# Kernel optimization log

Measured on AMD Instinct MI355X. Metric: run time of the kernel, lower is better.

## Reference

```python
import jax, jax.numpy as jnp
import numpy as np

# Static taxonomy layout (closed over; mirrors __init__ args La/layers)
LAYER_SIZES = (100, 1000, 5000, 13900)
LAYER_STARTS = tuple(int(s) for s in np.cumsum((0,) + LAYER_SIZES)[:-1])
N_NODES = int(sum(LAYER_SIZES))
H = len(LAYER_SIZES)
BATCH = 4096


def setup_inputs() -> dict:
    key = jax.random.key(0)
    y_pred = jax.random.normal(key, (BATCH, N_NODES), dtype=jnp.float32)

    rng = np.random.default_rng(0)
    # parents[v] = global index of v's parent in the previous layer
    parents = np.zeros(N_NODES, np.int32)
    for l in range(1, H):
        s, n = LAYER_STARTS[l], LAYER_SIZES[l]
        ps, pn = LAYER_STARTS[l - 1], LAYER_SIZES[l - 1]
        parents[s:s + n] = rng.integers(ps, ps + pn, size=n)

    # hierarchy-consistent one-hot targets: pick a leaf, mark it and all ancestors
    leaf = rng.integers(LAYER_STARTS[H - 1], N_NODES, size=BATCH)
    y_true = np.zeros((BATCH, N_NODES), np.float32)
    node = leaf
    rows = np.arange(BATCH)
    for l in range(H - 1, 0, -1):
        y_true[rows, node] = 1.0
        node = parents[node]
    y_true[rows, node] = 1.0  # layer-0 ancestor

    alpha_layer = jnp.array([0.0, 1.0, 1.0, 1.0], dtype=jnp.float32)
    return {
        "y_pred": y_pred,
        "y_true": jnp.asarray(y_true),
        "parents": jnp.asarray(parents),
        "alpha_layer": alpha_layer,
    }


def reference(y_pred, y_true, parents, alpha_layer):
    # Fused, batched version of the per-sample / per-layer Python loops.
    loss = jnp.float32(0.0)
    for l in range(1, H):  # small static loop over taxonomy layers
        s, n = LAYER_STARTS[l], LAYER_SIZES[l]
        ps, pn = LAYER_STARTS[l - 1], LAYER_SIZES[l - 1]

        logits = y_pred[:, s:s + n]                      # [B, n_l]
        p = jax.nn.softmax(logits, axis=1)               # outer softmax (as in source)
        # nn.CrossEntropyLoss with probability targets == -sum(t * log_softmax(input));
        # the source feeds the already-softmaxed p (double softmax) -> reproduce exactly.
        cce = -jnp.sum(y_true[:, s:s + n] * jax.nn.log_softmax(p, axis=1), axis=1)  # [B]

        # hierarchical dependency: child prob must not exceed its parent's prob
        pp = jax.nn.softmax(y_pred[:, ps:ps + pn], axis=1)   # [B, n_{l-1}]
        pidx = parents[s:s + n] - ps                         # local parent ids [n_l]
        d = jnp.mean(jax.nn.relu(p - pp[:, pidx]), axis=1)   # [B]

        loss = loss + jnp.mean(cce + d) * alpha_layer[l]
    return loss
```

## Files before the change

kernel.cpp:

```cpp
#include <hip/hip_runtime.h>
#include <math.h>

#define BATCH   4096
#define N_NODES 20000
#define H       4
#define BLOCK   512
#define NW      (BLOCK / 64)

__device__ __forceinline__ float waveSum(float v) {
#pragma unroll
    for (int off = 32; off > 0; off >>= 1) v += __shfl_xor(v, off);
    return v;
}

__device__ __forceinline__ ushort f2bf(float x) {
    unsigned u = __float_as_uint(x);
    u = (u + 0x7FFFu + ((u >> 16) & 1u)) >> 16;
    return (ushort)u;
}
__device__ __forceinline__ float bf2f(ushort h) {
    return __uint_as_float(((unsigned)h) << 16);
}

__device__ __forceinline__ void mzMerge(float& m, float& z, float m2, float z2) {
    float mn = fmaxf(m, m2);
    z = z * __expf(m - mn) + z2 * __expf(m2 - mn);
    m = mn;
}

__global__ __launch_bounds__(BLOCK, 8) void tax_main(
    const float* __restrict__ y_pred,
    const float* __restrict__ y_true,
    const int*   __restrict__ parents,
    const float* __restrict__ alpha,
    float*       __restrict__ partial)
{
    constexpr int LSTART[H] = {0, 100, 1100, 6100};
    constexpr int LSIZE[H]  = {100, 1000, 5000, 13900};

    __shared__ __align__(8) ushort row_bf[N_NODES];
    __shared__ float sc[112];
    __shared__ float m_s[H], invZ_s[H];

    const int tid = threadIdx.x;
    const int b   = blockIdx.x;
    const int wid = tid >> 6;
    const int lid = tid & 63;

    const float4* src4 = reinterpret_cast<const float4*>(y_pred + (size_t)b * N_NODES);

    float mL[H], zL[H];
#pragma unroll
    for (int l = 0; l < H; ++l) { mL[l] = -1e30f; zL[l] = 0.f; }

#pragma unroll
    for (int l = 0; l < H; ++l) {
        const int sq = LSTART[l] / 4, nq = LSIZE[l] / 4;
        for (int i = tid; i < nq; i += BLOCK) {
            float4 v = src4[sq + i];
            ushort4 h;
            h.x = f2bf(v.x); h.y = f2bf(v.y); h.z = f2bf(v.z); h.w = f2bf(v.w);
            *reinterpret_cast<ushort4*>(&row_bf[4 * (sq + i)]) = h;
            float qm = fmaxf(fmaxf(v.x, v.y), fmaxf(v.z, v.w));
            float mn = fmaxf(mL[l], qm);
            zL[l] = zL[l] * __expf(mL[l] - mn)
                  + __expf(v.x - mn) + __expf(v.y - mn)
                  + __expf(v.z - mn) + __expf(v.w - mn);
            mL[l] = mn;
        }
    }

#pragma unroll
    for (int l = 0; l < H; ++l) {
#pragma unroll
        for (int off = 32; off > 0; off >>= 1) {
            float m2 = __shfl_xor(mL[l], off);
            float z2 = __shfl_xor(zL[l], off);
            mzMerge(mL[l], zL[l], m2, z2);
        }
    }
    if (lid == 0) {
#pragma unroll
        for (int l = 0; l < H; ++l) {
            sc[wid * 8 + l * 2]     = mL[l];
            sc[wid * 8 + l * 2 + 1] = zL[l];
        }
    }
    __syncthreads();
    if (tid < H) {
        float m = -1e30f, z = 0.f;
        for (int w = 0; w < NW; ++w)
            mzMerge(m, z, sc[w * 8 + tid * 2], sc[w * 8 + tid * 2 + 1]);
        m_s[tid]    = m;
        invZ_s[tid] = 1.f / z;
    }
    __syncthreads();

#pragma unroll
    for (int l = 1; l < H; ++l) {
        const int s = LSTART[l], nq = LSIZE[l] / 4;
        const float invZ  = invZ_s[l],     m  = m_s[l];
        const float invZp = invZ_s[l - 1], mp = m_s[l - 1];
        const float4* yt4 = reinterpret_cast<const float4*>(y_true + (size_t)b * N_NODES + s);
        const int4*   pa4 = reinterpret_cast<const int4*>(parents + s);

        float S = 0.f, dot = 0.f, D = 0.f, yts = 0.f;
        for (int i = tid; i < nq; i += BLOCK) {
            ushort4 yh = *reinterpret_cast<const ushort4*>(&row_bf[s + 4 * i]);
            float4  yt = yt4[i];
            int4    pa = pa4[i];
            float p0 = __expf(bf2f(yh.x) - m) * invZ;
            float p1 = __expf(bf2f(yh.y) - m) * invZ;
            float p2 = __expf(bf2f(yh.z) - m) * invZ;
            float p3 = __expf(bf2f(yh.w) - m) * invZ;
            float pp0 = __expf(bf2f(row_bf[pa.x]) - mp) * invZp;
            float pp1 = __expf(bf2f(row_bf[pa.y]) - mp) * invZp;
            float pp2 = __expf(bf2f(row_bf[pa.z]) - mp) * invZp;
            float pp3 = __expf(bf2f(row_bf[pa.w]) - mp) * invZp;
            S   += __expf(p0) + __expf(p1) + __expf(p2) + __expf(p3);
            dot += yt.x * p0 + yt.y * p1 + yt.z * p2 + yt.w * p3;
            yts += yt.x + yt.y + yt.z + yt.w;
            D += fmaxf(p0 - pp0, 0.f) + fmaxf(p1 - pp1, 0.f)
               + fmaxf(p2 - pp2, 0.f) + fmaxf(p3 - pp3, 0.f);
        }

        S = waveSum(S); dot = waveSum(dot); D = waveSum(D); yts = waveSum(yts);
        if (lid == 0) {
            sc[wid * 12 + (l - 1) * 4 + 0] = S;
            sc[wid * 12 + (l - 1) * 4 + 1] = dot;
            sc[wid * 12 + (l - 1) * 4 + 2] = D;
            sc[wid * 12 + (l - 1) * 4 + 3] = yts;
        }
    }
    __syncthreads();

    if (tid < 12) {
        float a = 0.f;
        for (int w = 0; w < NW; ++w) a += sc[w * 12 + tid];
        sc[96 + tid] = a;
    }
    __syncthreads();

    if (tid == 0) {
        float loss = 0.f;
#pragma unroll
        for (int l = 1; l < H; ++l) {
            float S   = sc[96 + (l - 1) * 4 + 0];
            float dot = sc[96 + (l - 1) * 4 + 1];
            float D   = sc[96 + (l - 1) * 4 + 2];
            float yts = sc[96 + (l - 1) * 4 + 3];
            loss += alpha[l] * (logf(S) * yts - dot + D / (float)LSIZE[l]);
        }
        partial[b] = loss;
    }
}

__global__ __launch_bounds__(1024) void tax_reduce(
    const float* __restrict__ partial, float* __restrict__ out)
{
    __shared__ float red[16];
    const int tid = threadIdx.x, wid = tid >> 6, lid = tid & 63;
    float v = 0.f;
    for (int i = tid; i < BATCH; i += 1024) v += partial[i];
    v = waveSum(v);
    if (lid == 0) red[wid] = v;
    __syncthreads();
    if (wid == 0) {
        float x = (lid < 16) ? red[lid] : 0.f;
        x = waveSum(x);
        if (lid == 0) out[0] = x * (1.0f / (float)BATCH);
    }
}

extern "C" void kernel_launch(void* const* d_in, const int* in_sizes, int n_in,
                              void* d_out, int out_size, void* d_ws, size_t ws_size,
                              hipStream_t stream) {
    const float* y_pred  = (const float*)d_in[0];
    const float* y_true  = (const float*)d_in[1];
    const int*   parents = (const int*)d_in[2];
    const float* alpha   = (const float*)d_in[3];
    float* partial = (float*)d_ws;
    float* out     = (float*)d_out;

    tax_main<<<dim3(BATCH), dim3(BLOCK), 0, stream>>>(y_pred, y_true, parents, alpha, partial);
    tax_reduce<<<dim3(1), dim3(1024), 0, stream>>>(partial, out);
}
```

Before: 130.1 us.

## Fold y_true dot product into first streaming pass with online rescaling

The y_true row is now read during the first pass over y_pred. The target-weighted dot product of unnormalized exponentials is accumulated with the same online max rescaling used for the softmax denominator, then multiplied by 1/Z at the end. This removes the y_true global reads and the dot/yts accumulation from the second pass, so that pass only reads shared memory and parents. The same DRAM bytes are still read, but they are issued earlier and together with y_pred loads. The cost is extra registers and extra multiply-adds in the first pass.

```diff
diff --git a/kernel.cpp b/kernel.cpp
--- a/kernel.cpp
+++ b/kernel.cpp
@@ -22,12 +22,6 @@
     return __uint_as_float(((unsigned)h) << 16);
 }
 
-__device__ __forceinline__ void mzMerge(float& m, float& z, float m2, float z2) {
-    float mn = fmaxf(m, m2);
-    z = z * __expf(m - mn) + z2 * __expf(m2 - mn);
-    m = mn;
-}
-
 __global__ __launch_bounds__(BLOCK, 8) void tax_main(
     const float* __restrict__ y_pred,
     const float* __restrict__ y_true,
@@ -39,75 +33,97 @@
     constexpr int LSIZE[H]  = {100, 1000, 5000, 13900};
 
     __shared__ __align__(8) ushort row_bf[N_NODES];
-    __shared__ float sc[112];
-    __shared__ float m_s[H], invZ_s[H];
+    __shared__ float sc[128];
+    __shared__ float fin[6];
+    __shared__ float m_s[H], invZ_s[H], dot_s[H], yts_s[H];
 
     const int tid = threadIdx.x;
     const int b   = blockIdx.x;
     const int wid = tid >> 6;
     const int lid = tid & 63;
 
-    const float4* src4 = reinterpret_cast<const float4*>(y_pred + (size_t)b * N_NODES);
+    const float4* yp4 = reinterpret_cast<const float4*>(y_pred + (size_t)b * N_NODES);
+    const float4* yt4 = reinterpret_cast<const float4*>(y_true + (size_t)b * N_NODES);
 
-    float mL[H], zL[H];
+    float mL[H], zL[H], dotL[H], ytsL[H];
 #pragma unroll
-    for (int l = 0; l < H; ++l) { mL[l] = -1e30f; zL[l] = 0.f; }
+    for (int l = 0; l < H; ++l) { mL[l] = -1e30f; zL[l] = 0.f; dotL[l] = 0.f; ytsL[l] = 0.f; }
 
 #pragma unroll
     for (int l = 0; l < H; ++l) {
         const int sq = LSTART[l] / 4, nq = LSIZE[l] / 4;
+        float m = mL[l], z = zL[l], dt = dotL[l], ys = ytsL[l];
         for (int i = tid; i < nq; i += BLOCK) {
-            float4 v = src4[sq + i];
+            float4 v = yp4[sq + i];
             ushort4 h;
             h.x = f2bf(v.x); h.y = f2bf(v.y); h.z = f2bf(v.z); h.w = f2bf(v.w);
             *reinterpret_cast<ushort4*>(&row_bf[4 * (sq + i)]) = h;
             float qm = fmaxf(fmaxf(v.x, v.y), fmaxf(v.z, v.w));
-            float mn = fmaxf(mL[l], qm);
-            zL[l] = zL[l] * __expf(mL[l] - mn)
-                  + __expf(v.x - mn) + __expf(v.y - mn)
-                  + __expf(v.z - mn) + __expf(v.w - mn);
-            mL[l] = mn;
+            float mn = fmaxf(m, qm);
+            float a  = __expf(m - mn);
+            float e0 = __expf(v.x - mn), e1 = __expf(v.y - mn);
+            float e2 = __expf(v.z - mn), e3 = __expf(v.w - mn);
+            z = z * a + (e0 + e1) + (e2 + e3);
+            if (l > 0) {
+                float4 t = yt4[sq + i];
+                dt = dt * a + t.x * e0 + t.y * e1 + t.z * e2 + t.w * e3;
+                ys += (t.x + t.y) + (t.z + t.w);
+            }
+            m = mn;
         }
+        mL[l] = m; zL[l] = z; dotL[l] = dt; ytsL[l] = ys;
     }
 
 #pragma unroll
     for (int l = 0; l < H; ++l) {
+        float m = mL[l], z = zL[l], dt = dotL[l], ys = ytsL[l];
 #pragma unroll
         for (int off = 32; off > 0; off >>= 1) {
-            float m2 = __shfl_xor(mL[l], off);
-            float z2 = __shfl_xor(zL[l], off);
-            mzMerge(mL[l], zL[l], m2, z2);
+            float m2 = __shfl_xor(m, off), z2 = __shfl_xor(z, off);
+            float d2 = __shfl_xor(dt, off), y2 = __shfl_xor(ys, off);
+            float mn = fmaxf(m, m2);
+            float aa = __expf(m - mn), bb = __expf(m2 - mn);
+            z = z * aa + z2 * bb;
+            dt = dt * aa + d2 * bb;
+            m = mn; ys += y2;
         }
-    }
-    if (lid == 0) {
-#pragma unroll
-        for (int l = 0; l < H; ++l) {
-            sc[wid * 8 + l * 2]     = mL[l];
-            sc[wid * 8 + l * 2 + 1] = zL[l];
+        if (lid == 0) {
+            sc[wid * 16 + l * 4 + 0] = m;
+            sc[wid * 16 + l * 4 + 1] = z;
+            sc[wid * 16 + l * 4 + 2] = dt;
+            sc[wid * 16 + l * 4 + 3] = ys;
         }
     }
     __syncthreads();
+
     if (tid < H) {
-        float m = -1e30f, z = 0.f;
-        for (int w = 0; w < NW; ++w)
-            mzMerge(m, z, sc[w * 8 + tid * 2], sc[w * 8 + tid * 2 + 1]);
+        float m = -1e30f, z = 0.f, dt = 0.f, ys = 0.f;
+        for (int w = 0; w < NW; ++w) {
+            float m2 = sc[w * 16 + tid * 4 + 0], z2 = sc[w * 16 + tid * 4 + 1];
+            float d2 = sc[w * 16 + tid * 4 + 2], y2 = sc[w * 16 + tid * 4 + 3];
+            float mn = fmaxf(m, m2);
+            float aa = __expf(m - mn), bb = __expf(m2 - mn);
+            z = z * aa + z2 * bb;
+            dt = dt * aa + d2 * bb;
+            m = mn; ys += y2;
+        }
         m_s[tid]    = m;
         invZ_s[tid] = 1.f / z;
+        dot_s[tid]  = dt;
+        yts_s[tid]  = ys;
     }
     __syncthreads();
 
 #pragma unroll
     for (int l = 1; l < H; ++l) {
         const int s = LSTART[l], nq = LSIZE[l] / 4;
-        const float invZ  = invZ_s[l],     m  = m_s[l];
-        const float invZp = invZ_s[l - 1], mp = m_s[l - 1];
-        const float4* yt4 = reinterpret_cast<const float4*>(y_true + (size_t)b * N_NODES + s);
-        const int4*   pa4 = reinterpret_cast<const int4*>(parents + s);
+        const float m  = m_s[l],     invZ  = invZ_s[l];
+        const float mp = m_s[l - 1], invZp = invZ_s[l - 1];
+        const int4* pa4 = reinterpret_cast<const int4*>(parents + s);
 
-        float S = 0.f, dot = 0.f, D = 0.f, yts = 0.f;
+        float S = 0.f, D = 0.f;
         for (int i = tid; i < nq; i += BLOCK) {
             ushort4 yh = *reinterpret_cast<const ushort4*>(&row_bf[s + 4 * i]);
-            float4  yt = yt4[i];
             int4    pa = pa4[i];
             float p0 = __expf(bf2f(yh.x) - m) * invZ;
             float p1 = __expf(bf2f(yh.y) - m) * invZ;
@@ -117,27 +133,23 @@
             float pp1 = __expf(bf2f(row_bf[pa.y]) - mp) * invZp;
             float pp2 = __expf(bf2f(row_bf[pa.z]) - mp) * invZp;
             float pp3 = __expf(bf2f(row_bf[pa.w]) - mp) * invZp;
-            S   += __expf(p0) + __expf(p1) + __expf(p2) + __expf(p3);
-            dot += yt.x * p0 + yt.y * p1 + yt.z * p2 + yt.w * p3;
-            yts += yt.x + yt.y + yt.z + yt.w;
+            S += (__expf(p0) + __expf(p1)) + (__expf(p2) + __expf(p3));
             D += fmaxf(p0 - pp0, 0.f) + fmaxf(p1 - pp1, 0.f)
                + fmaxf(p2 - pp2, 0.f) + fmaxf(p3 - pp3, 0.f);
         }
-
-        S = waveSum(S); dot = waveSum(dot); D = waveSum(D); yts = waveSum(yts);
+        S = waveSum(S); D = waveSum(D);
         if (lid == 0) {
-            sc[wid * 12 + (l - 1) * 4 + 0] = S;
-            sc[wid * 12 + (l - 1) * 4 + 1] = dot;
-            sc[wid * 12 + (l - 1) * 4 + 2] = D;
-            sc[wid * 12 + (l - 1) * 4 + 3] = yts;
+            sc[wid * 8 + (l - 1)]     = S;
+            sc[wid * 8 + 4 + (l - 1)] = D;
         }
     }
     __syncthreads();
 
-    if (tid < 12) {
+    if (tid < 6) {
+        int lm = tid % 3, isD = tid / 3;
         float a = 0.f;
-        for (int w = 0; w < NW; ++w) a += sc[w * 12 + tid];
-        sc[96 + tid] = a;
+        for (int w = 0; w < NW; ++w) a += sc[w * 8 + isD * 4 + lm];
+        fin[tid] = a;
     }
     __syncthreads();
 
@@ -145,11 +157,10 @@
         float loss = 0.f;
 #pragma unroll
         for (int l = 1; l < H; ++l) {
-            float S   = sc[96 + (l - 1) * 4 + 0];
-            float dot = sc[96 + (l - 1) * 4 + 1];
-            float D   = sc[96 + (l - 1) * 4 + 2];
-            float yts = sc[96 + (l - 1) * 4 + 3];
-            loss += alpha[l] * (logf(S) * yts - dot + D / (float)LSIZE[l]);
+            float S   = fin[l - 1];
+            float D   = fin[3 + l - 1];
+            float dot = dot_s[l] * invZ_s[l];
+            loss += alpha[l] * (logf(S) * yts_s[l] - dot + D / (float)LSIZE[l]);
         }
         partial[b] = loss;
     }
```

After: 135.2 us. +3.9%, slower.
